# Kernel tuning notes

Measured on AMD Instinct MI355X. Metric: run time of the kernel, lower is better.

Reference implementation:

```python
import jax, jax.numpy as jnp
import numpy as np
import math

L, B = 1024, 256
SEQ_DIM, KMER_DIM, HID = 16, 256, 64
N_LAYERS = 2
IN_DIM = SEQ_DIM + KMER_DIM + 21  # 293


def _normalize(v, eps=1e-12):
    return v / jnp.maximum(jnp.linalg.norm(v, axis=-1, keepdims=True), eps)


def _nerf_rot(a, b, c):
    # rotation matrix with columns [bc, n x bc, n] from last three backbone points
    bc = _normalize(c - b)
    n = _normalize(jnp.cross(b - a, bc))
    return jnp.stack([bc, jnp.cross(n, bc), n], axis=-1)  # (..., 3, 3)


def pnerf(c_tilde, nfrag):
    # c_tilde: (3L, B, 3) SRF coordinates; parallelized natural extension of reference frame
    Ltot, batch = c_tilde.shape[0], c_tilde.shape[1]
    k = Ltot // nfrag
    # contiguous fragments of length k, folded into the batch dim: (k, nfrag*B, 3)
    x = c_tilde.reshape(nfrag, k, batch, 3).transpose(1, 0, 2, 3).reshape(k, nfrag * batch, 3)
    init = jnp.array([[-math.sqrt(0.5), math.sqrt(1.5), 0.0],
                      [-math.sqrt(2.0), 0.0, 0.0],
                      [0.0, 0.0, 0.0]], dtype=c_tilde.dtype)
    F = nfrag * batch
    carry0 = (jnp.broadcast_to(init[0], (F, 3)),
              jnp.broadcast_to(init[1], (F, 3)),
              jnp.broadcast_to(init[2], (F, 3)))

    def extend(carry, ct):
        a, b, c = carry
        R = _nerf_rot(a, b, c)                      # (F, 3, 3)
        d = c + jnp.einsum('fij,fj->fi', R, ct)     # (F, 3)
        return (b, c, d), d

    _, frag = jax.lax.scan(extend, carry0, x)        # (k, F, 3)
    frag = frag.reshape(k, nfrag, batch, 3).transpose(1, 0, 2, 3)  # (nfrag, k, B, 3)

    # assemble fragments sequentially; init frame is identity/origin so frag 0 passes through
    carryA = (jnp.broadcast_to(init[0], (batch, 3)),
              jnp.broadcast_to(init[1], (batch, 3)),
              jnp.broadcast_to(init[2], (batch, 3)))

    def assemble(carry, fr):
        a, b, c = carry
        R = _nerf_rot(a, b, c)                      # (B, 3, 3)
        y = c + jnp.einsum('bij,kbj->kbi', R, fr)   # (k, B, 3)
        return (y[-3], y[-2], y[-1]), y

    _, ys = jax.lax.scan(assemble, carryA, frag)     # (nfrag, k, B, 3)
    return ys.reshape(nfrag * k, batch, 3)


def setup_inputs() -> dict:
    key = jax.random.key(0)
    ks = jax.random.split(key, 12)
    s = 0.05
    return {
        'seq': jax.random.randint(ks[0], (L, B), 0, 20, dtype=jnp.int64),
        'kmer': jax.random.randint(ks[1], (L, B), 0, 22 ** 3, dtype=jnp.int64),
        'pssm': jax.random.uniform(ks[2], (L, B, 21), dtype=jnp.float32),
        'length': jax.random.randint(ks[3], (L,), 1, L, dtype=jnp.int64),
        'seq_embed': jax.random.normal(ks[4], (20, SEQ_DIM), dtype=jnp.float32) * s,
        'kmer_embed': jax.random.normal(ks[5], (22 ** 3, KMER_DIM), dtype=jnp.float32) * s,
        'W0': jax.random.normal(ks[6], (IN_DIM, HID), dtype=jnp.float32) * s,
        'b0': jnp.zeros((HID,), dtype=jnp.float32),
        'We': jax.random.normal(ks[7], (HID, HID), dtype=jnp.float32) * s,
        'be': jnp.zeros((HID,), dtype=jnp.float32),
        'W1': jax.random.normal(ks[8], (HID, 9), dtype=jnp.float32) * s,
        'b1': jnp.zeros((9,), dtype=jnp.float32),
    }


def reference(seq, kmer, pssm, length, seq_embed, kmer_embed, W0, b0, We, be, W1, b1):
    s = seq_embed[seq]                                   # (L, B, 16)
    km = kmer_embed[kmer]                                # (L, B, 256)
    h = jnp.concatenate([s, km, pssm], axis=2)           # (L, B, 293)
    h = h @ W0 + b0                                      # (L, B, 64)
    # torch list-multiplication shares the SAME Linear across the n_layers blocks
    for _ in range(N_LAYERS):
        h = jax.nn.relu(h @ We + be)                     # dropout is identity at eval
    srf = h @ W1 + b1                                    # (L, B, 9)
    Ld, Bd = srf.shape[0], srf.shape[1]
    srf = srf.reshape(Ld, Bd, 3, 3).transpose(0, 2, 1, 3).reshape(3 * Ld, Bd, 3)
    return pnerf(srf, int(math.sqrt(Ld)))
```

## Files before the change

kernel.cpp:

```cpp
#include <hip/hip_runtime.h>
#include <math.h>

typedef short bf16x8 __attribute__((ext_vector_type(8)));
typedef float f32x4  __attribute__((ext_vector_type(4)));

__device__ __forceinline__ unsigned short f2bf(float x) {
    unsigned int u = __float_as_uint(x);
    return (unsigned short)((u + 0x7FFFu + ((u >> 16) & 1u)) >> 16);
}
__device__ __forceinline__ float bf2f(unsigned short h) {
    return __uint_as_float(((unsigned int)h) << 16);
}
__device__ __forceinline__ void split2(float x, unsigned short& h, unsigned short& l) {
    h = f2bf(x);
    l = f2bf(x - bf2f(h));
}
__device__ __forceinline__ void split2t(float x, unsigned short& h, unsigned short& l) {
    unsigned int u = __float_as_uint(x);
    h = (unsigned short)(u >> 16);
    float r = x - __uint_as_float(u & 0xFFFF0000u);
    l = f2bf(r);
}

__device__ __forceinline__ int hsw(int row, int col) {
    return (row << 6) + ((((col >> 3) ^ (row & 7)) << 3) | (col & 7));
}

__device__ __forceinline__ float inv_norm3(float x, float y, float z) {
    float d = fmaf(x, x, fmaf(y, y, z * z));
    return rsqrtf(fmaxf(d, 1e-24f));
}
__device__ __forceinline__ float3 f3sub(float3 a, float3 b) {
    return make_float3(a.x - b.x, a.y - b.y, a.z - b.z);
}
__device__ __forceinline__ float3 f3cross(float3 a, float3 b) {
    return make_float3(a.y * b.z - a.z * b.y,
                       a.z * b.x - a.x * b.z,
                       a.x * b.y - a.y * b.x);
}
__device__ __forceinline__ void nerf_frame(const float3& A, const float3& Bv,
                                           const float3& C, float3& bc,
                                           float3& n, float3& m3) {
    float3 w  = f3sub(C, Bv);
    float3 v  = f3sub(Bv, A);
    float3 cr = f3cross(v, w);
    float iw = inv_norm3(w.x, w.y, w.z);
    float ic = inv_norm3(cr.x, cr.y, cr.z);
    bc = make_float3(w.x * iw, w.y * iw, w.z * iw);
    n  = make_float3(cr.x * ic, cr.y * ic, cr.z * ic);
    m3 = f3cross(n, bc);
}
__device__ __forceinline__ float3 nerf_place(const float3& C, const float3& bc,
                                             const float3& m3, const float3& n,
                                             float tx, float ty, float tz) {
    return make_float3(
        fmaf(m3.x, ty, fmaf(bc.x, tx, fmaf(n.x, tz, C.x))),
        fmaf(m3.y, ty, fmaf(bc.y, tx, fmaf(n.y, tz, C.y))),
        fmaf(m3.z, ty, fmaf(bc.z, tx, fmaf(n.z, tz, C.z))));
}

struct KParams {
    const int* seq; const int* kmer; const float* pssm;
    const float* se; const float* emb;
    const float* W0; const float* b0; const float* We; const float* be;
    const float* W1; const float* b1;
    float* kmerT; float* seqT; float* srf_t; float* fragbuf;
    float4* frames; float* FPbuf; float* out;
    unsigned short *WeTH, *WeTL, *W0pTH, *W0pTL, *W1TH, *W1TL;
};

__global__ __launch_bounds__(256) void tables_kernel(KParams P) {
    const int tid = threadIdx.x;
    const int vb  = blockIdx.x;
    if (vb < 167) {
        const int lane = tid & 63;
        const int wv   = __builtin_amdgcn_readfirstlane(tid >> 6);
        const int q    = lane >> 4;
        const int c16  = lane & 15;
        const int r0   = vb * 64;
        const int n    = wv * 16 + c16;

        bf16x8 BH[8], BL[8];
        #pragma unroll
        for (int kt8 = 0; kt8 < 8; ++kt8)
            #pragma unroll
            for (int j = 0; j < 8; ++j) {
                float w = P.W0[(16 + kt8 * 32 + q * 8 + j) * 64 + n];
                unsigned short h, l; split2t(w, h, l);
                BH[kt8][j] = (short)h; BL[kt8][j] = (short)l;
            }
        f32x4 acc[4];
        #pragma unroll
        for (int t = 0; t < 4; ++t) acc[t] = (f32x4){0.f, 0.f, 0.f, 0.f};
        #pragma unroll
        for (int kt8 = 0; kt8 < 8; ++kt8) {
            #pragma unroll
            for (int t = 0; t < 4; ++t) {
                int rr = r0 + t * 16 + c16;
                if (rr > 10647) rr = 10647;
                const float* ap = P.emb + rr * 256 + kt8 * 32 + q * 8;
                float4 a0 = *(const float4*)ap;
                float4 a1 = *(const float4*)(ap + 4);
                bf16x8 ah, al;
                unsigned short h, l;
                split2t(a0.x, h, l); ah[0] = (short)h; al[0] = (short)l;
                split2t(a0.y, h, l); ah[1] = (short)h; al[1] = (short)l;
                split2t(a0.z, h, l); ah[2] = (short)h; al[2] = (short)l;
                split2t(a0.w, h, l); ah[3] = (short)h; al[3] = (short)l;
                split2t(a1.x, h, l); ah[4] = (short)h; al[4] = (short)l;
                split2t(a1.y, h, l); ah[5] = (short)h; al[5] = (short)l;
                split2t(a1.z, h, l); ah[6] = (short)h; al[6] = (short)l;
                split2t(a1.w, h, l); ah[7] = (short)h; al[7] = (short)l;
                acc[t] = __builtin_amdgcn_mfma_f32_16x16x32_bf16(ah, BH[kt8], acc[t], 0, 0, 0);
                acc[t] = __builtin_amdgcn_mfma_f32_16x16x32_bf16(al, BH[kt8], acc[t], 0, 0, 0);
                acc[t] = __builtin_amdgcn_mfma_f32_16x16x32_bf16(ah, BL[kt8], acc[t], 0, 0, 0);
            }
        }
        #pragma unroll
        for (int t = 0; t < 4; ++t)
            #pragma unroll
            for (int r = 0; r < 4; ++r) {
                int row = r0 + t * 16 + q * 4 + r;
                if (row < 10648) P.kmerT[row * 64 + n] = acc[t][r];
            }
    } else if (vb < 172) {
        int e = (vb - 167) * 256 + tid;
        int r = e >> 6, j = e & 63;
        float acc = P.b0[j];
        #pragma unroll
        for (int k = 0; k < 16; ++k)
            acc = fmaf(P.se[r * 16 + k], P.W0[k * 64 + j], acc);
        float cs = 0.f;
        #pragma unroll
        for (int c = 0; c < 21; ++c) cs += P.W0[(272 + c) * 64 + j];
        P.seqT[r * 64 + j] = acc + 0.5f * cs;
    } else {
        #pragma unroll
        for (int i = 0; i < 16; ++i) {
            int e = i * 256 + tid;
            int k = e >> 6, n = e & 63;
            unsigned short h, l; split2(P.We[k * 64 + n], h, l);
            P.WeTH[n * 64 + k] = h; P.WeTL[n * 64 + k] = l;
        }
        #pragma unroll
        for (int i = 0; i < 8; ++i) {
            int e = i * 256 + tid;
            int k = e >> 6, n = e & 63;
            float w = (k < 21) ? P.W0[(272 + k) * 64 + n] : 0.f;
            unsigned short h, l; split2(w, h, l);
            P.W0pTH[n * 32 + k] = h; P.W0pTL[n * 32 + k] = l;
        }
        #pragma unroll
        for (int i = 0; i < 4; ++i) {
            int e = i * 256 + tid;
            int k = e >> 4, c = e & 15;
            float w = (c < 9) ? P.W1[k * 9 + c] : 0.f;
            unsigned short h, l; split2(w, h, l);
            P.W1TH[c * 64 + k] = h; P.W1TL[c * 64 + k] = l;
        }
    }
}

__global__ __launch_bounds__(256, 4) void mlp_kernel(KParams P) {
    __shared__ __align__(16) unsigned char SMEM[32768];
    unsigned short* Hah = (unsigned short*)(SMEM);
    unsigned short* Hal = (unsigned short*)(SMEM + 8192);
    unsigned short* Hbh = (unsigned short*)(SMEM + 16384);
    unsigned short* Hbl = (unsigned short*)(SMEM + 24576);
    unsigned short (*Ph)[40] = (unsigned short (*)[40])(SMEM + 16384);
    unsigned short (*Pl)[40] = (unsigned short (*)[40])(SMEM + 16384 + 5120);

    const int tid  = threadIdx.x;
    const int lane = tid & 63;
    const int wv   = __builtin_amdgcn_readfirstlane(tid >> 6);
    const int q    = lane >> 4;
    const int c16  = lane & 15;
    const int m0   = blockIdx.x * 64;
    const int n    = wv * 16 + c16;

    const int mypack = P.seq[m0 + lane] | (P.kmer[m0 + lane] << 5);
    float g[4][4];
    #pragma unroll
    for (int t = 0; t < 4; ++t)
        #pragma unroll
        for (int r = 0; r < 4; ++r) {
            int src = (t * 16 + q * 4 + r) << 2;
            int v   = __builtin_amdgcn_ds_bpermute(src, mypack);
            int s   = v & 31;
            int km  = v >> 5;
            g[t][r] = P.seqT[s * 64 + n] + P.kmerT[km * 64 + n];
        }

    for (int i = tid; i < 64 * 21; i += 256) {
        float v = P.pssm[m0 * 21 + i] - 0.5f;
        unsigned short h, l; split2t(v, h, l);
        Ph[i / 21][i % 21] = h;
        Pl[i / 21][i % 21] = l;
    }
    for (int i = tid; i < 64 * 11; i += 256) {
        Ph[i / 11][21 + (i % 11)] = 0;
        Pl[i / 11][21 + (i % 11)] = 0;
    }

    bf16x8 WeH[2], WeL[2], W1H[2], W1L[2], W0H, W0L;
    #pragma unroll
    for (int kk = 0; kk < 2; ++kk) {
        WeH[kk] = *(const bf16x8*)(P.WeTH + n * 64 + kk * 32 + q * 8);
        WeL[kk] = *(const bf16x8*)(P.WeTL + n * 64 + kk * 32 + q * 8);
        W1H[kk] = *(const bf16x8*)(P.W1TH + c16 * 64 + kk * 32 + q * 8);
        W1L[kk] = *(const bf16x8*)(P.W1TL + c16 * 64 + kk * 32 + q * 8);
    }
    W0H = *(const bf16x8*)(P.W0pTH + n * 32 + q * 8);
    W0L = *(const bf16x8*)(P.W0pTL + n * 32 + q * 8);
    const float be_n = P.be[n];
    const float b1h  = (c16 < 9) ? P.b1[c16] : 0.f;
    __syncthreads();

    f32x4 acc[4];
    #pragma unroll
    for (int t = 0; t < 4; ++t) acc[t] = (f32x4){0.f, 0.f, 0.f, 0.f};
    #pragma unroll
    for (int t = 0; t < 4; ++t) {
        bf16x8 ah = *(const bf16x8*)&Ph[t * 16 + c16][q * 8];
        bf16x8 al = *(const bf16x8*)&Pl[t * 16 + c16][q * 8];
        acc[t] = __builtin_amdgcn_mfma_f32_16x16x32_bf16(ah, W0H, acc[t], 0, 0, 0);
        acc[t] = __builtin_amdgcn_mfma_f32_16x16x32_bf16(al, W0H, acc[t], 0, 0, 0);
        acc[t] = __builtin_amdgcn_mfma_f32_16x16x32_bf16(ah, W0L, acc[t], 0, 0, 0);
    }
    #pragma unroll
    for (int t = 0; t < 4; ++t)
        #pragma unroll
        for (int r = 0; r < 4; ++r) {
            unsigned short h, l; split2t(acc[t][r] + g[t][r], h, l);
            Hah[hsw(t * 16 + q * 4 + r, n)] = h;
            Hal[hsw(t * 16 + q * 4 + r, n)] = l;
        }
    __syncthreads();

    {
        f32x4 a1[4];
        #pragma unroll
        for (int t = 0; t < 4; ++t) {
            a1[t] = (f32x4){be_n, be_n, be_n, be_n};
            #pragma unroll
            for (int kk = 0; kk < 2; ++kk) {
                bf16x8 ah = *(const bf16x8*)&Hah[hsw(t * 16 + c16, kk * 32 + q * 8)];
                bf16x8 al = *(const bf16x8*)&Hal[hsw(t * 16 + c16, kk * 32 + q * 8)];
                a1[t] = __builtin_amdgcn_mfma_f32_16x16x32_bf16(ah, WeH[kk], a1[t], 0, 0, 0);
                a1[t] = __builtin_amdgcn_mfma_f32_16x16x32_bf16(al, WeH[kk], a1[t], 0, 0, 0);
                a1[t] = __builtin_amdgcn_mfma_f32_16x16x32_bf16(ah, WeL[kk], a1[t], 0, 0, 0);
            }
        }
        #pragma unroll
        for (int t = 0; t < 4; ++t)
            #pragma unroll
            for (int r = 0; r < 4; ++r) {
                unsigned short h, l; split2t(fmaxf(a1[t][r], 0.f), h, l);
                Hbh[hsw(t * 16 + q * 4 + r, n)] = h;
                Hbl[hsw(t * 16 + q * 4 + r, n)] = l;
            }
        __syncthreads();
    }
    {
        f32x4 a2[4];
        #pragma unroll
        for (int t = 0; t < 4; ++t) {
            a2[t] = (f32x4){be_n, be_n, be_n, be_n};
            #pragma unroll
            for (int kk = 0; kk < 2; ++kk) {
                bf16x8 ah = *(const bf16x8*)&Hbh[hsw(t * 16 + c16, kk * 32 + q * 8)];
                bf16x8 al = *(const bf16x8*)&Hbl[hsw(t * 16 + c16, kk * 32 + q * 8)];
                a2[t] = __builtin_amdgcn_mfma_f32_16x16x32_bf16(ah, WeH[kk], a2[t], 0, 0, 0);
                a2[t] = __builtin_amdgcn_mfma_f32_16x16x32_bf16(al, WeH[kk], a2[t], 0, 0, 0);
                a2[t] = __builtin_amdgcn_mfma_f32_16x16x32_bf16(ah, WeL[kk], a2[t], 0, 0, 0);
            }
        }
        #pragma unroll
        for (int t = 0; t < 4; ++t)
            #pragma unroll
            for (int r = 0; r < 4; ++r) {
                unsigned short h, l; split2t(fmaxf(a2[t][r], 0.f), h, l);
                Hah[hsw(t * 16 + q * 4 + r, n)] = h;
                Hal[hsw(t * 16 + q * 4 + r, n)] = l;
            }
        __syncthreads();
    }
    {
        f32x4 ah4 = (f32x4){b1h, b1h, b1h, b1h};
        #pragma unroll
        for (int kk = 0; kk < 2; ++kk) {
            bf16x8 ah = *(const bf16x8*)&Hah[hsw(wv * 16 + c16, kk * 32 + q * 8)];
            bf16x8 al = *(const bf16x8*)&Hal[hsw(wv * 16 + c16, kk * 32 + q * 8)];
            ah4 = __builtin_amdgcn_mfma_f32_16x16x32_bf16(ah, W1H[kk], ah4, 0, 0, 0);
            ah4 = __builtin_amdgcn_mfma_f32_16x16x32_bf16(al, W1H[kk], ah4, 0, 0, 0);
            ah4 = __builtin_amdgcn_mfma_f32_16x16x32_bf16(ah, W1L[kk], ah4, 0, 0, 0);
        }
        if (c16 < 9) {
            #pragma unroll
            for (int r = 0; r < 4; ++r) {
                int pos = m0 + wv * 16 + q * 4 + r;
                int l = pos >> 8, b = pos & 255;
                P.srf_t[(l * 9 + c16) * 256 + b] = ah4[r];
            }
        }
    }
}

__global__ __launch_bounds__(64) void extend_kernel(KParams P) {
    int frag = blockIdx.x >> 2;
    int bb   = ((blockIdx.x & 3) << 6) + threadIdx.x;

    float3 A  = make_float3(-0.70710678118654752f, 1.22474487139158905f, 0.f);
    float3 Bv = make_float3(-1.41421356237309505f, 0.f, 0.f);
    float3 C  = make_float3(0.f, 0.f, 0.f);

    float ct0[9], ct1[9], ct2[9], ct3[9];
    #pragma unroll
    for (int m = 0; m < 9; ++m) {
        ct0[m] = P.srf_t[((frag * 32 + 0) * 9 + m) * 256 + bb];
        ct1[m] = P.srf_t[((frag * 32 + 1) * 9 + m) * 256 + bb];
        ct2[m] = P.srf_t[((frag * 32 + 2) * 9 + m) * 256 + bb];
    }
    for (int ll = 0; ll < 32; ++ll) {
        if (ll < 29) {
            #pragma unroll
            for (int m = 0; m < 9; ++m)
                ct3[m] = P.srf_t[((frag * 32 + ll + 3) * 9 + m) * 256 + bb];
        } else {
            #pragma unroll
            for (int m = 0; m < 9; ++m) ct3[m] = 0.f;
        }
        #pragma unroll
        for (int s3 = 0; s3 < 3; ++s3) {
            float3 bc, nn, m3;
            nerf_frame(A, Bv, C, bc, nn, m3);
            float3 d = nerf_place(C, bc, m3, nn,
                                  ct0[3 * s3 + 0], ct0[3 * s3 + 1], ct0[3 * s3 + 2]);
            int row = frag * 96 + ll * 3 + s3;
            P.fragbuf[(row * 3 + 0) * 256 + bb] = d.x;
            P.fragbuf[(row * 3 + 1) * 256 + bb] = d.y;
            P.fragbuf[(row * 3 + 2) * 256 + bb] = d.z;
            A = Bv; Bv = C; C = d;
        }
        #pragma unroll
        for (int m = 0; m < 9; ++m) { ct0[m] = ct1[m]; ct1[m] = ct2[m]; ct2[m] = ct3[m]; }
    }
    float3 bc, nn, m3;
    nerf_frame(A, Bv, C, bc, nn, m3);
    P.FPbuf[(frag * 12 + 0)  * 256 + bb] = bc.x;
    P.FPbuf[(frag * 12 + 1)  * 256 + bb] = bc.y;
    P.FPbuf[(frag * 12 + 2)  * 256 + bb] = bc.z;
    P.FPbuf[(frag * 12 + 3)  * 256 + bb] = m3.x;
    P.FPbuf[(frag * 12 + 4)  * 256 + bb] = m3.y;
    P.FPbuf[(frag * 12 + 5)  * 256 + bb] = m3.z;
    P.FPbuf[(frag * 12 + 6)  * 256 + bb] = nn.x;
    P.FPbuf[(frag * 12 + 7)  * 256 + bb] = nn.y;
    P.FPbuf[(frag * 12 + 8)  * 256 + bb] = nn.z;
    P.FPbuf[(frag * 12 + 9)  * 256 + bb] = C.x;
    P.FPbuf[(frag * 12 + 10) * 256 + bb] = C.y;
    P.FPbuf[(frag * 12 + 11) * 256 + bb] = C.z;
}

__global__ __launch_bounds__(256) void carry_kernel(KParams P) {
    __shared__ float S[384][16];
    const int tid  = threadIdx.x;
    const int base = blockIdx.x * 16;
    for (int i = tid; i < 384 * 16; i += 256) {
        int row = i >> 4, col = i & 15;
        S[row][col] = P.FPbuf[row * 256 + base + col];
    }
    __syncthreads();
    if (tid < 16) {
        int bb = base + tid;
        float3 ob = make_float3(1.f, 0.f, 0.f);
        float3 om = make_float3(0.f, 1.f, 0.f);
        float3 on = make_float3(0.f, 0.f, 1.f);
        float3 c  = make_float3(0.f, 0.f, 0.f);
        for (int f = 0; f < 32; ++f) {
            int fb = (f * 256 + bb) * 3;
            P.frames[fb + 0] = make_float4(ob.x, ob.y, ob.z, om.x);
            P.frames[fb + 1] = make_float4(om.y, om.z, on.x, on.y);
            P.frames[fb + 2] = make_float4(on.z, c.x, c.y, c.z);

            int r0 = f * 12;
            float3 Fb = make_float3(S[r0+0][tid], S[r0+1][tid], S[r0+2][tid]);
            float3 Fm = make_float3(S[r0+3][tid], S[r0+4][tid], S[r0+5][tid]);
            float3 Fn = make_float3(S[r0+6][tid], S[r0+7][tid], S[r0+8][tid]);
            float3 p  = make_float3(S[r0+9][tid], S[r0+10][tid], S[r0+11][tid]);

            float3 nb = make_float3(
                fmaf(ob.x,Fb.x, fmaf(om.x,Fb.y, on.x*Fb.z)),
                fmaf(ob.y,Fb.x, fmaf(om.y,Fb.y, on.y*Fb.z)),
                fmaf(ob.z,Fb.x, fmaf(om.z,Fb.y, on.z*Fb.z)));
            float3 nm = make_float3(
                fmaf(ob.x,Fm.x, fmaf(om.x,Fm.y, on.x*Fm.z)),
                fmaf(ob.y,Fm.x, fmaf(om.y,Fm.y, on.y*Fm.z)),
                fmaf(ob.z,Fm.x, fmaf(om.z,Fm.y, on.z*Fm.z)));
            float3 nn2 = make_float3(
                fmaf(ob.x,Fn.x, fmaf(om.x,Fn.y, on.x*Fn.z)),
                fmaf(ob.y,Fn.x, fmaf(om.y,Fn.y, on.y*Fn.z)),
                fmaf(ob.z,Fn.x, fmaf(om.z,Fn.y, on.z*Fn.z)));
            float3 nc = make_float3(
                fmaf(ob.x,p.x, fmaf(om.x,p.y, fmaf(on.x,p.z, c.x))),
                fmaf(ob.y,p.x, fmaf(om.y,p.y, fmaf(on.y,p.z, c.y))),
                fmaf(ob.z,p.x, fmaf(om.z,p.y, fmaf(on.z,p.z, c.z))));
            ob = nb; om = nm; on = nn2; c = nc;
        }
    }
}

__global__ __launch_bounds__(256) void apply_kernel(KParams P) {
    __shared__ float sm[768];
    const int bb = threadIdx.x;
    #pragma unroll 1
    for (int i = 0; i < 4; ++i) {
        const int row  = blockIdx.x * 4 + i;
        const int frag = row / 96;

        float fx = P.fragbuf[(row * 3 + 0) * 256 + bb];
        float fy = P.fragbuf[(row * 3 + 1) * 256 + bb];
        float fz = P.fragbuf[(row * 3 + 2) * 256 + bb];

        int fb = (frag * 256 + bb) * 3;
        float4 f0 = P.frames[fb + 0];
        float4 f1 = P.frames[fb + 1];
        float4 f2 = P.frames[fb + 2];

        float ox = f2.y + f0.x * fx + f0.w * fy + f1.z * fz;
        float oy = f2.z + f0.y * fx + f1.x * fy + f1.w * fz;
        float oz = f2.w + f0.z * fx + f1.y * fy + f2.x * fz;

        __syncthreads();
        sm[bb * 3 + 0] = ox;
        sm[bb * 3 + 1] = oy;
        sm[bb * 3 + 2] = oz;
        __syncthreads();

        int base = row * 768;
        P.out[base + bb]       = sm[bb];
        P.out[base + 256 + bb] = sm[256 + bb];
        P.out[base + 512 + bb] = sm[512 + bb];
    }
}

extern "C" void kernel_launch(void* const* d_in, const int* in_sizes, int n_in,
                              void* d_out, int out_size, void* d_ws, size_t ws_size,
                              hipStream_t stream) {
    float* ws      = (float*)d_ws;
    float* kmerT   = ws;
    float* seqT    = kmerT + 681472;
    float* srf_t   = seqT + 1280;
    float* fragbuf = srf_t + 2359296;
    float* frames  = fragbuf + 2359296;
    float* FPbuf   = frames + 98304;

    unsigned short* WeTH  = (unsigned short*)fragbuf;
    unsigned short* WeTL  = WeTH + 4096;
    unsigned short* W0pTH = WeTL + 4096;
    unsigned short* W0pTL = W0pTH + 2048;
    unsigned short* W1TH  = W0pTL + 2048;
    unsigned short* W1TL  = W1TH + 1024;

    KParams P;
    P.seq  = (const int*)d_in[0];
    P.kmer = (const int*)d_in[1];
    P.pssm = (const float*)d_in[2];
    P.se   = (const float*)d_in[4];
    P.emb  = (const float*)d_in[5];
    P.W0   = (const float*)d_in[6];
    P.b0   = (const float*)d_in[7];
    P.We   = (const float*)d_in[8];
    P.be   = (const float*)d_in[9];
    P.W1   = (const float*)d_in[10];
    P.b1   = (const float*)d_in[11];
    P.kmerT = kmerT; P.seqT = seqT; P.srf_t = srf_t; P.fragbuf = fragbuf;
    P.frames = (float4*)frames; P.FPbuf = FPbuf; P.out = (float*)d_out;
    P.WeTH = WeTH; P.WeTL = WeTL; P.W0pTH = W0pTH; P.W0pTL = W0pTL;
    P.W1TH = W1TH; P.W1TL = W1TL;

    hipLaunchKernelGGL(tables_kernel, dim3(173),  dim3(256), 0, stream, P);
    hipLaunchKernelGGL(mlp_kernel,    dim3(4096), dim3(256), 0, stream, P);
    hipLaunchKernelGGL(extend_kernel, dim3(128),  dim3(64),  0, stream, P);
    hipLaunchKernelGGL(carry_kernel,  dim3(16),   dim3(256), 0, stream, P);
    hipLaunchKernelGGL(apply_kernel,  dim3(768),  dim3(256), 0, stream, P);
}
```

Baseline: 175.7 us.

## Process two 64-row tiles per MLP block to amortize weight loads and barriers

```diff
diff --git a/kernel.cpp b/kernel.cpp
--- a/kernel.cpp
+++ b/kernel.cpp
@@ -161,45 +161,54 @@
     }
 }
 
-__global__ __launch_bounds__(256, 4) void mlp_kernel(KParams P) {
-    __shared__ __align__(16) unsigned char SMEM[32768];
-    unsigned short* Hah = (unsigned short*)(SMEM);
-    unsigned short* Hal = (unsigned short*)(SMEM + 8192);
-    unsigned short* Hbh = (unsigned short*)(SMEM + 16384);
-    unsigned short* Hbl = (unsigned short*)(SMEM + 24576);
-    unsigned short (*Ph)[40] = (unsigned short (*)[40])(SMEM + 16384);
-    unsigned short (*Pl)[40] = (unsigned short (*)[40])(SMEM + 16384 + 5120);
+__global__ __launch_bounds__(256, 2) void mlp_kernel(KParams P) {
+    __shared__ __align__(16) unsigned char SMEM[65536];
 
     const int tid  = threadIdx.x;
     const int lane = tid & 63;
     const int wv   = __builtin_amdgcn_readfirstlane(tid >> 6);
     const int q    = lane >> 4;
     const int c16  = lane & 15;
-    const int m0   = blockIdx.x * 64;
+    const int m0   = blockIdx.x * 128;
     const int n    = wv * 16 + c16;
 
-    const int mypack = P.seq[m0 + lane] | (P.kmer[m0 + lane] << 5);
-    float g[4][4];
-    #pragma unroll
-    for (int t = 0; t < 4; ++t)
-        #pragma unroll
-        for (int r = 0; r < 4; ++r) {
-            int src = (t * 16 + q * 4 + r) << 2;
-            int v   = __builtin_amdgcn_ds_bpermute(src, mypack);
-            int s   = v & 31;
-            int km  = v >> 5;
-            g[t][r] = P.seqT[s * 64 + n] + P.kmerT[km * 64 + n];
-        }
-
-    for (int i = tid; i < 64 * 21; i += 256) {
-        float v = P.pssm[m0 * 21 + i] - 0.5f;
-        unsigned short h, l; split2t(v, h, l);
-        Ph[i / 21][i % 21] = h;
-        Pl[i / 21][i % 21] = l;
-    }
-    for (int i = tid; i < 64 * 11; i += 256) {
-        Ph[i / 11][21 + (i % 11)] = 0;
-        Pl[i / 11][21 + (i % 11)] = 0;
+    unsigned short* Hah[2] = {(unsigned short*)(SMEM),
+                             (unsigned short*)(SMEM + 32768)};
+    unsigned short* Hal[2] = {(unsigned short*)(SMEM + 8192),
+                             (unsigned short*)(SMEM + 40960)};
+    unsigned short* Hbh[2] = {(unsigned short*)(SMEM + 16384),
+                             (unsigned short*)(SMEM + 49152)};
+    unsigned short* Hbl[2] = {(unsigned short*)(SMEM + 24576),
+                             (unsigned short*)(SMEM + 57344)};
+
+    float g[2][4][4];
+    #pragma unroll
+    for (int u = 0; u < 2; ++u) {
+        const int mypack = P.seq[m0 + u * 64 + lane] | (P.kmer[m0 + u * 64 + lane] << 5);
+        #pragma unroll
+        for (int t = 0; t < 4; ++t)
+            #pragma unroll
+            for (int r = 0; r < 4; ++r) {
+                int src = (t * 16 + q * 4 + r) << 2;
+                int v   = __builtin_amdgcn_ds_bpermute(src, mypack);
+                g[u][t][r] = P.seqT[(v & 31) * 64 + n] + P.kmerT[(v >> 5) * 64 + n];
+            }
+    }
+
+    #pragma unroll
+    for (int u = 0; u < 2; ++u) {
+        unsigned short (*Ph)[40] = (unsigned short (*)[40])(Hbh[u]);
+        unsigned short (*Pl)[40] = (unsigned short (*)[40])((unsigned char*)Hbh[u] + 5120);
+        for (int i = tid; i < 64 * 21; i += 256) {
+            float v = P.pssm[(m0 + u * 64) * 21 + i] - 0.5f;
+            unsigned short h, l; split2t(v, h, l);
+            Ph[i / 21][i % 21] = h;
+            Pl[i / 21][i % 21] = l;
+        }
+        for (int i = tid; i < 64 * 11; i += 256) {
+            Ph[i / 11][21 + (i % 11)] = 0;
+            Pl[i / 11][21 + (i % 11)] = 0;
+        }
     }
 
     bf16x8 WeH[2], WeL[2], W1H[2], W1L[2], W0H, W0L;
@@ -216,36 +225,42 @@
     const float b1h  = (c16 < 9) ? P.b1[c16] : 0.f;
     __syncthreads();
 
-    f32x4 acc[4];
-    #pragma unroll
-    for (int t = 0; t < 4; ++t) acc[t] = (f32x4){0.f, 0.f, 0.f, 0.f};
-    #pragma unroll
-    for (int t = 0; t < 4; ++t) {
-        bf16x8 ah = *(const bf16x8*)&Ph[t * 16 + c16][q * 8];
-        bf16x8 al = *(const bf16x8*)&Pl[t * 16 + c16][q * 8];
-        acc[t] = __builtin_amdgcn_mfma_f32_16x16x32_bf16(ah, W0H, acc[t], 0, 0, 0);
-        acc[t] = __builtin_amdgcn_mfma_f32_16x16x32_bf16(al, W0H, acc[t], 0, 0, 0);
-        acc[t] = __builtin_amdgcn_mfma_f32_16x16x32_bf16(ah, W0L, acc[t], 0, 0, 0);
-    }
-    #pragma unroll
-    for (int t = 0; t < 4; ++t)
-        #pragma unroll
-        for (int r = 0; r < 4; ++r) {
-            unsigned short h, l; split2t(acc[t][r] + g[t][r], h, l);
-            Hah[hsw(t * 16 + q * 4 + r, n)] = h;
-            Hal[hsw(t * 16 + q * 4 + r, n)] = l;
-        }
+    #pragma unroll
+    for (int u = 0; u < 2; ++u) {
+        unsigned short (*Ph)[40] = (unsigned short (*)[40])(Hbh[u]);
+        unsigned short (*Pl)[40] = (unsigned short (*)[40])((unsigned char*)Hbh[u] + 5120);
+        f32x4 acc[4];
+        #pragma unroll
+        for (int t = 0; t < 4; ++t) acc[t] = (f32x4){0.f, 0.f, 0.f, 0.f};
+        #pragma unroll
+        for (int t = 0; t < 4; ++t) {
+            bf16x8 ah = *(const bf16x8*)&Ph[t * 16 + c16][q * 8];
+            bf16x8 al = *(const bf16x8*)&Pl[t * 16 + c16][q * 8];
+            acc[t] = __builtin_amdgcn_mfma_f32_16x16x32_bf16(ah, W0H, acc[t], 0, 0, 0);
+            acc[t] = __builtin_amdgcn_mfma_f32_16x16x32_bf16(al, W0H, acc[t], 0, 0, 0);
+            acc[t] = __builtin_amdgcn_mfma_f32_16x16x32_bf16(ah, W0L, acc[t], 0, 0, 0);
+        }
+        #pragma unroll
+        for (int t = 0; t < 4; ++t)
+            #pragma unroll
+            for (int r = 0; r < 4; ++r) {
+                unsigned short h, l; split2t(acc[t][r] + g[u][t][r], h, l);
+                Hah[u][hsw(t * 16 + q * 4 + r, n)] = h;
+                Hal[u][hsw(t * 16 + q * 4 + r, n)] = l;
+            }
+    }
     __syncthreads();
 
-    {
+    #pragma unroll
+    for (int u = 0; u < 2; ++u) {
         f32x4 a1[4];
         #pragma unroll
         for (int t = 0; t < 4; ++t) {
             a1[t] = (f32x4){be_n, be_n, be_n, be_n};
             #pragma unroll
             for (int kk = 0; kk < 2; ++kk) {
-                bf16x8 ah = *(const bf16x8*)&Hah[hsw(t * 16 + c16, kk * 32 + q * 8)];
-                bf16x8 al = *(const bf16x8*)&Hal[hsw(t * 16 + c16, kk * 32 + q * 8)];
+                bf16x8 ah = *(const bf16x8*)&Hah[u][hsw(t * 16 + c16, kk * 32 + q * 8)];
+                bf16x8 al = *(const bf16x8*)&Hal[u][hsw(t * 16 + c16, kk * 32 + q * 8)];
                 a1[t] = __builtin_amdgcn_mfma_f32_16x16x32_bf16(ah, WeH[kk], a1[t], 0, 0, 0);
                 a1[t] = __builtin_amdgcn_mfma_f32_16x16x32_bf16(al, WeH[kk], a1[t], 0, 0, 0);
                 a1[t] = __builtin_amdgcn_mfma_f32_16x16x32_bf16(ah, WeL[kk], a1[t], 0, 0, 0);
@@ -256,20 +271,22 @@
             #pragma unroll
             for (int r = 0; r < 4; ++r) {
                 unsigned short h, l; split2t(fmaxf(a1[t][r], 0.f), h, l);
-                Hbh[hsw(t * 16 + q * 4 + r, n)] = h;
-                Hbl[hsw(t * 16 + q * 4 + r, n)] = l;
-            }
-        __syncthreads();
-    }
-    {
+                Hbh[u][hsw(t * 16 + q * 4 + r, n)] = h;
+                Hbl[u][hsw(t * 16 + q * 4 + r, n)] = l;
+            }
+    }
+    __syncthreads();
+
+    #pragma unroll
+    for (int u = 0; u < 2; ++u) {
         f32x4 a2[4];
         #pragma unroll
         for (int t = 0; t < 4; ++t) {
             a2[t] = (f32x4){be_n, be_n, be_n, be_n};
             #pragma unroll
             for (int kk = 0; kk < 2; ++kk) {
-                bf16x8 ah = *(const bf16x8*)&Hbh[hsw(t * 16 + c16, kk * 32 + q * 8)];
-                bf16x8 al = *(const bf16x8*)&Hbl[hsw(t * 16 + c16, kk * 32 + q * 8)];
+                bf16x8 ah = *(const bf16x8*)&Hbh[u][hsw(t * 16 + c16, kk * 32 + q * 8)];
+                bf16x8 al = *(const bf16x8*)&Hbl[u][hsw(t * 16 + c16, kk * 32 + q * 8)];
                 a2[t] = __builtin_amdgcn_mfma_f32_16x16x32_bf16(ah, WeH[kk], a2[t], 0, 0, 0);
                 a2[t] = __builtin_amdgcn_mfma_f32_16x16x32_bf16(al, WeH[kk], a2[t], 0, 0, 0);
                 a2[t] = __builtin_amdgcn_mfma_f32_16x16x32_bf16(ah, WeL[kk], a2[t], 0, 0, 0);
@@ -280,17 +297,19 @@
             #pragma unroll
             for (int r = 0; r < 4; ++r) {
                 unsigned short h, l; split2t(fmaxf(a2[t][r], 0.f), h, l);
-                Hah[hsw(t * 16 + q * 4 + r, n)] = h;
-                Hal[hsw(t * 16 + q * 4 + r, n)] = l;
-            }
-        __syncthreads();
-    }
-    {
+                Hah[u][hsw(t * 16 + q * 4 + r, n)] = h;
+                Hal[u][hsw(t * 16 + q * 4 + r, n)] = l;
+            }
+    }
+    __syncthreads();
+
+    #pragma unroll
+    for (int u = 0; u < 2; ++u) {
         f32x4 ah4 = (f32x4){b1h, b1h, b1h, b1h};
         #pragma unroll
         for (int kk = 0; kk < 2; ++kk) {
-            bf16x8 ah = *(const bf16x8*)&Hah[hsw(wv * 16 + c16, kk * 32 + q * 8)];
-            bf16x8 al = *(const bf16x8*)&Hal[hsw(wv * 16 + c16, kk * 32 + q * 8)];
+            bf16x8 ah = *(const bf16x8*)&Hah[u][hsw(wv * 16 + c16, kk * 32 + q * 8)];
+            bf16x8 al = *(const bf16x8*)&Hal[u][hsw(wv * 16 + c16, kk * 32 + q * 8)];
             ah4 = __builtin_amdgcn_mfma_f32_16x16x32_bf16(ah, W1H[kk], ah4, 0, 0, 0);
             ah4 = __builtin_amdgcn_mfma_f32_16x16x32_bf16(al, W1H[kk], ah4, 0, 0, 0);
             ah4 = __builtin_amdgcn_mfma_f32_16x16x32_bf16(ah, W1L[kk], ah4, 0, 0, 0);
@@ -298,7 +317,7 @@
         if (c16 < 9) {
             #pragma unroll
             for (int r = 0; r < 4; ++r) {
-                int pos = m0 + wv * 16 + q * 4 + r;
+                int pos = m0 + u * 64 + wv * 16 + q * 4 + r;
                 int l = pos >> 8, b = pos & 255;
                 P.srf_t[(l * 9 + c16) * 256 + b] = ah4[r];
             }
@@ -479,7 +498,7 @@
     P.W1TH = W1TH; P.W1TL = W1TL;
 
     hipLaunchKernelGGL(tables_kernel, dim3(173),  dim3(256), 0, stream, P);
-    hipLaunchKernelGGL(mlp_kernel,    dim3(4096), dim3(256), 0, stream, P);
+    hipLaunchKernelGGL(mlp_kernel,    dim3(2048), dim3(256), 0, stream, P);
     hipLaunchKernelGGL(extend_kernel, dim3(128),  dim3(64),  0, stream, P);
     hipLaunchKernelGGL(carry_kernel,  dim3(16),   dim3(256), 0, stream, P);
     hipLaunchKernelGGL(apply_kernel,  dim3(768),  dim3(256), 0, stream, P);
```

After: 186.8 us. 1.06x slower.
